# Optimization experiments

Measured on AMD Instinct MI355X. Metric: run time of the kernel, lower is better.

Reference implementation:

```python
import jax, jax.numpy as jnp
import numpy as np

N_NODE, N_PRICE, N_CB, N_CM = 50000, 100, 50, 500
EMB, NNZ, LAYERS = 128, 1_000_000, 2


def setup_inputs() -> dict:
    key = jax.random.key(0)
    ks = iter(jax.random.split(key, 64))
    f = lambda shape: jax.random.normal(next(ks), shape, dtype=jnp.float32)
    u = lambda shape: jax.random.uniform(next(ks), shape, dtype=jnp.float32)
    inp = {
        'adj_indices': jax.random.randint(next(ks), (2, NNZ), 0, N_NODE),
        'adj_values': u((NNZ,)),
        'adjacency_pv': u((N_PRICE, N_NODE)),
        'adjacency_vp': u((N_NODE, N_PRICE)),
        'adjacency_pcb': u((N_PRICE, N_CB)),
        'adjacency_cbp': u((N_CB, N_PRICE)),
        'adjacency_cbv': u((N_CB, N_NODE)),
        'adjacency_vcb': u((N_NODE, N_CB)),
        'adjacency_pcm': u((N_PRICE, N_CM)),
        'adjacency_cmp': u((N_CM, N_PRICE)),
        'adjacency_cmv': u((N_CM, N_NODE)),
        'adjacency_vcm': u((N_NODE, N_CM)),
        'adjacency_cbcm': u((N_CB, N_CM)),
        'adjacency_cmcb': u((N_CM, N_CB)),
        'item_emb': f((N_NODE, EMB)) * 0.1,
        'pri_emb': f((N_PRICE, EMB)) * 0.1,
        'cateBig_emb': f((N_CB, EMB)) * 0.1,
        'cateMiddle_emb': f((N_CM, EMB)) * 0.1,
        'mat_vp': f((N_NODE, 1)), 'mat_vcb': f((N_NODE, 1)), 'mat_vcm': f((N_NODE, 1)),
        'mat_pv': f((N_PRICE, 1)), 'mat_pcb': f((N_PRICE, 1)), 'mat_pcm': f((N_PRICE, 1)),
        'mat_cbp': f((N_CB, 1)), 'mat_cbv': f((N_CB, 1)), 'mat_cbcm': f((N_CB, 1)),
        'mat_cmp': f((N_CM, 1)), 'mat_cmv': f((N_CM, 1)), 'mat_cmcb': f((N_CM, 1)),
        'Wi': f((EMB, 1)) * 0.1, 'bi': jnp.zeros((1,), jnp.float32),
        'Wp': f((EMB, 1)) * 0.1, 'bp': jnp.zeros((1,), jnp.float32),
        'Wcb': f((EMB, 1)) * 0.1, 'bcb': jnp.zeros((1,), jnp.float32),
        'Wcm': f((EMB, 1)) * 0.1, 'bcm': jnp.zeros((1,), jnp.float32),
    }
    return inp


def _intra_gate(dense_adj, mat_v, emb2):
    # original: alpha = softmax(mm(expand(mat_v), emb2^T)) == softmax(mat_v * rowsum(emb2))
    s = jnp.sum(emb2, axis=1)               # [m]
    alpha = jax.nn.softmax(mat_v * s[None, :], axis=1)  # [n,m] (mat_v is [n,1])
    alpha = alpha * dense_adj
    alpha = alpha / (jnp.sum(alpha, axis=1, keepdims=True) + 1e-8)
    return alpha @ emb2                      # [n,emb]  (dropout70 omitted: eval mode)


def _inter_gate(W, b, e0, e1, e2, e3):
    embs = (e0, e1, e2, e3)
    scores = [jnp.exp(e @ W + b) for e in embs]   # each [n,1]
    tot = scores[0] + scores[1] + scores[2] + scores[3]
    out = sum((s / tot) * e for s, e in zip(scores, embs))
    return out                               # (dropout50 omitted: eval mode)


def _spmm(indices, values, emb, num_rows):
    # sparse COO adjacency @ emb : out[row] += val * emb[col]
    return jax.ops.segment_sum(values[:, None] * emb[indices[1]], indices[0],
                               num_segments=num_rows)


def reference(adj_indices, adj_values,
              adjacency_pv, adjacency_vp, adjacency_pcb, adjacency_cbp,
              adjacency_cbv, adjacency_vcb, adjacency_pcm, adjacency_cmp,
              adjacency_cmv, adjacency_vcm, adjacency_cbcm, adjacency_cmcb,
              item_emb, pri_emb, cateBig_emb, cateMiddle_emb,
              mat_vp, mat_vcb, mat_vcm, mat_pv, mat_pcb, mat_pcm,
              mat_cbp, mat_cbv, mat_cbcm, mat_cmp, mat_cmv, mat_cmcb,
              Wi, bi, Wp, bp, Wcb, bcb, Wcm, bcm):
    for _ in range(LAYERS):
        item_new = _inter_gate(Wi, bi, item_emb,
                               _intra_gate(adjacency_vp, mat_vp, pri_emb),
                               _intra_gate(adjacency_vcb, mat_vcb, cateBig_emb),
                               _intra_gate(adjacency_vcm, mat_vcm, cateMiddle_emb)) \
                   + _spmm(adj_indices, adj_values, item_emb, N_NODE)
        pri_new = _inter_gate(Wp, bp, pri_emb,
                              _intra_gate(adjacency_pv, mat_pv, item_emb),
                              _intra_gate(adjacency_pcb, mat_pcb, cateBig_emb),
                              _intra_gate(adjacency_pcm, mat_pcm, cateMiddle_emb))
        cb_new = _inter_gate(Wcb, bcb, cateBig_emb,
                             _intra_gate(adjacency_cbp, mat_cbp, pri_emb),
                             _intra_gate(adjacency_cbv, mat_cbv, item_emb),
                             _intra_gate(adjacency_cbcm, mat_cbcm, cateMiddle_emb))
        cm_new = _inter_gate(Wcm, bcm, cateMiddle_emb,
                             _intra_gate(adjacency_cmp, mat_cmp, pri_emb),
                             _intra_gate(adjacency_cmv, mat_cmv, item_emb),
                             _intra_gate(adjacency_cmcb, mat_cmcb, cateBig_emb))
        item_emb, pri_emb, cateBig_emb, cateMiddle_emb = item_new, pri_new, cb_new, cm_new
    return (item_emb, pri_emb)
```

## Files before the change

### kernel.cpp

```cpp
#include <hip/hip_runtime.h>

#define N_NODE 50000
#define N_PRICE 100
#define N_CB 50
#define N_CM 500
#define EMB 128
#define NNZE 1000000
#define NCH 64
#define CS2 832
#define KVPAD 53248
#define RSTRIDE 132
#define SCAN_T 1024
#define WPAD 72
#define E0P 132

typedef __attribute__((ext_vector_type(8))) short bf16x8;
typedef __attribute__((ext_vector_type(4))) float f32x4;

__device__ inline unsigned fkey(float f){
    unsigned b = __float_as_uint(f);
    return (b & 0x80000000u) ? ~b : (b | 0x80000000u);
}
__device__ inline float fdekey(unsigned k){
    unsigned b = (k & 0x80000000u) ? (k & 0x7fffffffu) : ~k;
    return __uint_as_float(b);
}
__device__ inline unsigned short f2bf(float f){
    unsigned u = __float_as_uint(f);
    u += 0x7FFFu + ((u >> 16) & 1u);
    return (unsigned short)(u >> 16);
}

__global__ __launch_bounds__(256) void k_rowsum(
    const float* __restrict__ e_v, const float* __restrict__ e_p,
    const float* __restrict__ e_cb, const float* __restrict__ e_cm,
    float* __restrict__ s_all, unsigned* __restrict__ mm)
{
    if (blockIdx.x == 0 && threadIdx.x < 8)
        mm[threadIdx.x] = (threadIdx.x & 1) ? 0u : 0xFFFFFFFFu;
    int wid  = (blockIdx.x * 256 + threadIdx.x) >> 6;
    int lane = threadIdx.x & 63;
    const int NT = N_NODE + N_PRICE + N_CB + N_CM;
    if (wid >= NT) return;
    const float* src; int lr;
    if (wid < N_NODE)                { src = e_v;  lr = wid; }
    else if (wid < N_NODE+N_PRICE)   { src = e_p;  lr = wid - N_NODE; }
    else if (wid < N_NODE+N_PRICE+N_CB){ src = e_cb; lr = wid - N_NODE - N_PRICE; }
    else                             { src = e_cm; lr = wid - N_NODE - N_PRICE - N_CB; }
    float2 v = ((const float2*)(src + (size_t)lr * EMB))[lane];
    float sum = v.x + v.y;
    #pragma unroll
    for (int o = 32; o > 0; o >>= 1) sum += __shfl_down(sum, o, 64);
    if (lane == 0) s_all[wid] = sum;
}

__global__ __launch_bounds__(256) void k_minmax(
    const float* __restrict__ s_all, unsigned* __restrict__ mm)
{
    __shared__ unsigned smin[4], smax[4];
    int t = threadIdx.x;
    if (t < 4){ smin[t] = 0xFFFFFFFFu; smax[t] = 0u; }
    __syncthreads();
    int gid = blockIdx.x * 256 + t;
    const int NT = N_NODE + N_PRICE + N_CB + N_CM;
    if (gid < NT){
        int ty = (gid < N_NODE) ? 0 :
                 (gid < N_NODE+N_PRICE) ? 1 :
                 (gid < N_NODE+N_PRICE+N_CB) ? 2 : 3;
        unsigned k = fkey(s_all[gid]);
        atomicMin(&smin[ty], k);
        atomicMax(&smax[ty], k);
    }
    __syncthreads();
    if (t < 4){
        if (smin[t] != 0xFFFFFFFFu) atomicMin(&mm[2*t],   smin[t]);
        if (smax[t] != 0u)          atomicMax(&mm[2*t+1], smax[t]);
    }
}

__global__ __launch_bounds__(256) void k_hist(
    const int* __restrict__ rows, int* __restrict__ counts)
{
    int i = blockIdx.x * 256 + threadIdx.x;
    if (i < NNZE) atomicAdd(&counts[rows[i]], 1);
}

__global__ __launch_bounds__(SCAN_T) void k_scan(
    const int* __restrict__ counts, int* __restrict__ offs, int* __restrict__ cursor)
{
    __shared__ int part[SCAN_T];
    int t = threadIdx.x;
    const int CHUNK = (N_NODE + SCAN_T - 1) / SCAN_T;
    int base = t * CHUNK;
    int s = 0;
    for (int i = 0; i < CHUNK; i++){
        int idx = base + i;
        if (idx < N_NODE) s += counts[idx];
    }
    part[t] = s;
    __syncthreads();
    for (int o = 1; o < SCAN_T; o <<= 1){
        int u = (t >= o) ? part[t - o] : 0;
        __syncthreads();
        part[t] += u;
        __syncthreads();
    }
    int run = part[t] - s;
    for (int i = 0; i < CHUNK; i++){
        int idx = base + i;
        if (idx < N_NODE){
            offs[idx] = run; cursor[idx] = run;
            run += counts[idx];
        }
    }
    if (t == SCAN_T - 1) offs[N_NODE] = run;
}

__global__ __launch_bounds__(256) void k_scatter(
    const int* __restrict__ rows, const int* __restrict__ cols,
    const float* __restrict__ vals, int* __restrict__ cursor,
    int* __restrict__ scol, float* __restrict__ sval)
{
    int i = blockIdx.x * 256 + threadIdx.x;
    if (i < NNZE){
        int r = rows[i];
        int p = atomicAdd(&cursor[r], 1);
        scol[p] = cols[i];
        sval[p] = vals[i];
    }
}

__global__ __launch_bounds__(256) void k_spmm_csr(
    const int* __restrict__ offs, const int* __restrict__ scol,
    const float* __restrict__ sval, const float* __restrict__ emb,
    float* __restrict__ out)
{
    int row  = (blockIdx.x * 256 + threadIdx.x) >> 6;
    int lane = threadIdx.x & 63;
    if (row >= N_NODE) return;
    int s = offs[row], e = offs[row + 1];
    float2 acc = make_float2(0.f, 0.f);
    for (int base = s; base < e; base += 64){
        int n = base + lane;
        int   cl = (n < e) ? scol[n] : 0;
        float vl = (n < e) ? sval[n] : 0.f;
        int m = e - base; if (m > 64) m = 64;
        for (int j = 0; j < m; j++){
            int   c = __shfl(cl, j, 64);
            float v = __shfl(vl, j, 64);
            float2 em = *(const float2*)(emb + (size_t)c * EMB + lane * 2);
            acc.x += v * em.x; acc.y += v * em.y;
        }
    }
    float* dst = out + (size_t)row * EMB + lane * 2;
    float2 o = *(float2*)dst;
    o.x += acc.x; o.y += acc.y;
    *(float2*)dst = o;
}

__global__ __launch_bounds__(256) void k_cast_et_t(
    const float* __restrict__ emb, unsigned short* __restrict__ Et,
    int K, int Kpad)
{
    __shared__ unsigned short tl[64][72];
    int k0 = blockIdx.x * 64, d0 = blockIdx.y * 64;
    int t = threadIdx.x;
    int r = t >> 2, cb = (t & 3) * 16;
    const float* src = emb + (size_t)(k0 + r) * EMB + d0 + cb;
    bool rv = (k0 + r) < K;
    #pragma unroll
    for (int q = 0; q < 4; q++){
        float4 v = rv ? ((const float4*)src)[q] : make_float4(0.f,0.f,0.f,0.f);
        tl[r][cb + q*4 + 0] = f2bf(v.x);
        tl[r][cb + q*4 + 1] = f2bf(v.y);
        tl[r][cb + q*4 + 2] = f2bf(v.z);
        tl[r][cb + q*4 + 3] = f2bf(v.w);
    }
    __syncthreads();
    unsigned short h[16];
    #pragma unroll
    for (int j = 0; j < 16; j++) h[j] = tl[cb + j][r];
    uint4* dst = (uint4*)(Et + (size_t)(d0 + r) * Kpad + k0 + cb);
    dst[0] = make_uint4(((unsigned)h[1]<<16)|h[0], ((unsigned)h[3]<<16)|h[2],
                        ((unsigned)h[5]<<16)|h[4], ((unsigned)h[7]<<16)|h[6]);
    dst[1] = make_uint4(((unsigned)h[9]<<16)|h[8], ((unsigned)h[11]<<16)|h[10],
                        ((unsigned)h[13]<<16)|h[12],((unsigned)h[15]<<16)|h[14]);
}

__device__ inline void gate_block_mfma(
    const float* __restrict__ adj, const float* __restrict__ matv,
    const unsigned short* __restrict__ Et, const float* __restrict__ s_src,
    const unsigned* __restrict__ mm2, float* __restrict__ out,
    int K, int Kpad, int nrows, int i0,
    unsigned short* sh_w, float* sh_c, float* sh_M, float* shD, float* shZ)
{
    int tid = threadIdx.x;
    if (tid < 64){
        int i = i0 + tid;
        float c = (i < nrows) ? matv[i] : 0.f;
        float smin = fdekey(mm2[0]), smax = fdekey(mm2[1]);
        sh_c[tid] = c;
        sh_M[tid] = (c >= 0.f) ? c * smax : c * smin;
    }
    __syncthreads();

    int wv = tid >> 6, lane = tid & 63;
    int half = lane >> 5, c2 = (lane & 31) * 2;
    int am = lane & 15, aq = lane >> 4;

    unsigned roff[8];
    float crow[8], Mrow[8], zacc[8], dacc[8];
    #pragma unroll
    for (int i = 0; i < 8; i++){
        int r = wv*16 + i*2 + half;
        int ir = i0 + r; if (ir >= nrows) ir = nrows - 1;
        roff[i] = (unsigned)ir * (unsigned)K;
        crow[i] = sh_c[r]; Mrow[i] = sh_M[r];
        zacc[i] = 0.f; dacc[i] = 0.f;
    }
    f32x4 acc[8];
    #pragma unroll
    for (int n = 0; n < 8; n++) acc[n] = (f32x4){0.f,0.f,0.f,0.f};

    int ntile = Kpad / 64;
    for (int t = 0; t < ntile; t++){
        int k0 = t * 64;
        bool inb = (k0 + c2) < K;
        float2 s2 = inb ? *(const float2*)&s_src[k0 + c2] : make_float2(0.f,0.f);
        float2 av[8];
        #pragma unroll
        for (int i = 0; i < 8; i++)
            av[i] = inb ? *(const float2*)&adj[roff[i] + k0 + c2]
                        : make_float2(0.f, 0.f);
        __syncthreads();
        #pragma unroll
        for (int i = 0; i < 8; i++){
            float ex = 0.f, ey = 0.f;
            if (inb){
                ex = __expf(crow[i]*s2.x - Mrow[i]);
                ey = __expf(crow[i]*s2.y - Mrow[i]);
            }
            zacc[i] += ex + ey;
            float wx = ex * av[i].x, wy = ey * av[i].y;
            dacc[i] += wx + wy;
            *(unsigned*)&sh_w[(wv*16 + i*2 + half) * WPAD + c2] =
                (unsigned)f2bf(wx) | ((unsigned)f2bf(wy) << 16);
        }
        __syncthreads();
        #pragma unroll
        for (int ks = 0; ks < 2; ks++){
            bf16x8 afrag = *(const bf16x8*)&sh_w[(wv*16 + am) * WPAD + ks*32 + aq*8];
            #pragma unroll
            for (int n = 0; n < 8; n++){
                bf16x8 bfrag = *(const bf16x8*)&Et[(size_t)(n*16 + am) * Kpad + k0 + ks*32 + aq*8];
                acc[n] = __builtin_amdgcn_mfma_f32_16x16x32_bf16(afrag, bfrag, acc[n], 0, 0, 0);
            }
        }
    }
    #pragma unroll
    for (int o = 1; o <= 16; o <<= 1)
        #pragma unroll
        for (int i = 0; i < 8; i++){
            dacc[i] += __shfl_xor(dacc[i], o, 64);
            zacc[i] += __shfl_xor(zacc[i], o, 64);
        }
    if ((lane & 31) == 0){
        #pragma unroll
        for (int i = 0; i < 8; i++){
            shD[wv*16 + i*2 + half] = dacc[i];
            shZ[wv*16 + i*2 + half] = zacc[i];
        }
    }
    __syncthreads();
    #pragma unroll
    for (int n = 0; n < 8; n++){
        #pragma unroll
        for (int r = 0; r < 4; r++){
            int rl = wv*16 + aq*4 + r;
            int i  = i0 + rl;
            if (i < nrows){
                float inv = 1.f / (shD[rl] + 1e-8f * shZ[rl]);
                out[(size_t)i * EMB + n*16 + am] = acc[n][r] * inv;
            }
        }
    }
}

struct GateJob {
    const float* adj; const float* matv; const unsigned short* Et;
    const float* s; const unsigned* mm2; float* out;
    int K, Kpad, nrows, blk0;
};
struct GateJobs { GateJob j[6]; int njobs; };

__global__ __launch_bounds__(256) void k_gate_batch(GateJobs jobs)
{
    __shared__ unsigned short sh_w[64 * WPAD];
    __shared__ float sh_c[64], sh_M[64], shD[64], shZ[64];
    int b = blockIdx.x;
    int ji = 0;
    for (int q = 1; q < jobs.njobs; q++) if (b >= jobs.j[q].blk0) ji = q;
    GateJob J = jobs.j[ji];
    gate_block_mfma(J.adj, J.matv, J.Et, J.s, J.mm2, J.out, J.K, J.Kpad,
                    J.nrows, (b - J.blk0) * 64, sh_w, sh_c, sh_M, shD, shZ);
}

struct FGate {
    const float* adj; const float* matv; const unsigned short* Et;
    const unsigned* mm2; int K, Kpad, soff;
};
struct FParams { FGate g[3]; };

__global__ __launch_bounds__(256) void k_item_fused(
    FParams P, const float* __restrict__ cv, const float* __restrict__ sseg,
    const float* __restrict__ W, const float* __restrict__ bptr,
    float* __restrict__ out)
{
    __shared__ unsigned short sh_w[64 * WPAD];
    __shared__ float sh_e0[64 * E0P];
    __shared__ float shs[672];
    __shared__ float sh_c[3][64], sh_M[3][64];
    __shared__ float shD[64], shZ[64];
    __shared__ float shWf[128];

    int tid = threadIdx.x;
    int i0  = blockIdx.x * 64;

    for (int j = tid; j < 672; j += 256) shs[j] = (j < 650) ? sseg[j] : 0.f;
    if (tid < 128) shWf[tid] = W[tid];
    if (tid < 192){
        int g = tid >> 6, r = tid & 63;
        int i = i0 + r;
        float c = (i < N_NODE) ? P.g[g].matv[i] : 0.f;
        float smin = fdekey(P.g[g].mm2[0]), smax = fdekey(P.g[g].mm2[1]);
        sh_c[g][r] = c;
        sh_M[g][r] = (c >= 0.f) ? c * smax : c * smin;
    }
    for (int f = tid; f < 64 * 32; f += 256){
        int row = f >> 5, d4 = (f & 31) * 4;
        int i = i0 + row;
        float4 v = (i < N_NODE) ? ((const float4*)(cv + (size_t)i * EMB + d4))[0]
                                : make_float4(0.f,0.f,0.f,0.f);
        ((float4*)&sh_e0[row * E0P + d4])[0] = v;
    }
    __syncthreads();

    int wv = tid >> 6, lane = tid & 63;
    int half = lane >> 5, c2 = (lane & 31) * 2;
    int am = lane & 15, aq = lane >> 4;
    float bb = bptr[0];

    float dp[4] = {0.f,0.f,0.f,0.f};
    #pragma unroll
    for (int n = 0; n < 8; n++)
        #pragma unroll
        for (int r = 0; r < 4; r++)
            dp[r] += sh_e0[(wv*16 + aq*4 + r) * E0P + n*16 + am] * shWf[n*16 + am];
    #pragma unroll
    for (int o = 1; o <= 8; o <<= 1)
        #pragma unroll
        for (int r = 0; r < 4; r++) dp[r] += __shfl_xor(dp[r], o, 64);
    float stot[4];
    #pragma unroll
    for (int r = 0; r < 4; r++) stot[r] = __expf(dp[r] + bb);
    f32x4 run[8];
    #pragma unroll
    for (int n = 0; n < 8; n++)
        #pragma unroll
        for (int r = 0; r < 4; r++)
            run[n][r] = stot[r] * sh_e0[(wv*16 + aq*4 + r) * E0P + n*16 + am];

    for (int g = 0; g < 3; g++){
        FGate G = P.g[g];
        const float* srcs = shs + G.soff;
        unsigned roff[8];
        float crow[8], Mrow[8], zacc[8], dacc[8];
        #pragma unroll
        for (int i = 0; i < 8; i++){
            int r = wv*16 + i*2 + half;
            int ir = i0 + r; if (ir >= N_NODE) ir = N_NODE - 1;
            roff[i] = (unsigned)ir * (unsigned)G.K;
            crow[i] = sh_c[g][r]; Mrow[i] = sh_M[g][r];
            zacc[i] = 0.f; dacc[i] = 0.f;
        }
        f32x4 acc[8];
        #pragma unroll
        for (int n = 0; n < 8; n++) acc[n] = (f32x4){0.f,0.f,0.f,0.f};
        int ntile = G.Kpad >> 6;

        for (int t = 0; t < ntile; t++){
            int k0 = t * 64;
            bool inb = (k0 + c2) < G.K;
            float2 s2 = *(const float2*)&srcs[k0 + c2];
            float2 av[8];
            #pragma unroll
            for (int i = 0; i < 8; i++)
                av[i] = inb ? *(const float2*)&G.adj[roff[i] + k0 + c2]
                            : make_float2(0.f, 0.f);
            __syncthreads();
            #pragma unroll
            for (int i = 0; i < 8; i++){
                float ex = 0.f, ey = 0.f;
                if (inb){
                    ex = __expf(crow[i]*s2.x - Mrow[i]);
                    ey = __expf(crow[i]*s2.y - Mrow[i]);
                }
                zacc[i] += ex + ey;
                float wx = ex * av[i].x, wy = ey * av[i].y;
                dacc[i] += wx + wy;
                *(unsigned*)&sh_w[(wv*16 + i*2 + half) * WPAD + c2] =
                    (unsigned)f2bf(wx) | ((unsigned)f2bf(wy) << 16);
            }
            __syncthreads();
            #pragma unroll
            for (int ks = 0; ks < 2; ks++){
                bf16x8 afrag = *(const bf16x8*)&sh_w[(wv*16 + am) * WPAD + ks*32 + aq*8];
                #pragma unroll
                for (int n = 0; n < 8; n++){
                    bf16x8 bfrag = *(const bf16x8*)&G.Et[(size_t)(n*16 + am) * G.Kpad + k0 + ks*32 + aq*8];
                    acc[n] = __builtin_amdgcn_mfma_f32_16x16x32_bf16(afrag, bfrag, acc[n], 0, 0, 0);
                }
            }
        }
        #pragma unroll
        for (int o = 1; o <= 16; o <<= 1)
            #pragma unroll
            for (int i = 0; i < 8; i++){
                dacc[i] += __shfl_xor(dacc[i], o, 64);
                zacc[i] += __shfl_xor(zacc[i], o, 64);
            }
        if ((lane & 31) == 0){
            #pragma unroll
            for (int i = 0; i < 8; i++){
                shD[wv*16 + i*2 + half] = dacc[i];
                shZ[wv*16 + i*2 + half] = zacc[i];
            }
        }
        __syncthreads();
        float inv[4];
        #pragma unroll
        for (int r = 0; r < 4; r++){
            int rl = wv*16 + aq*4 + r;
            inv[r] = 1.f / (shD[rl] + 1e-8f * shZ[rl]);
        }
        float dpg[4] = {0.f,0.f,0.f,0.f};
        #pragma unroll
        for (int n = 0; n < 8; n++)
            #pragma unroll
            for (int r = 0; r < 4; r++){
                acc[n][r] *= inv[r];
                dpg[r] += acc[n][r] * shWf[n*16 + am];
            }
        #pragma unroll
        for (int o = 1; o <= 8; o <<= 1)
            #pragma unroll
            for (int r = 0; r < 4; r++) dpg[r] += __shfl_xor(dpg[r], o, 64);
        #pragma unroll
        for (int r = 0; r < 4; r++){
            float sg = __expf(dpg[r] + bb);
            stot[r] += sg;
            #pragma unroll
            for (int n = 0; n < 8; n++) run[n][r] += sg * acc[n][r];
        }
    }
    float invs[4];
    #pragma unroll
    for (int r = 0; r < 4; r++) invs[r] = 1.f / stot[r];
    #pragma unroll
    for (int n = 0; n < 8; n++)
        #pragma unroll
        for (int r = 0; r < 4; r++){
            int i = i0 + wv*16 + aq*4 + r;
            if (i < N_NODE) out[(size_t)i * EMB + n*16 + am] = run[n][r] * invs[r];
        }
}

__global__ __launch_bounds__(256) void k_intra_tv_mfma(
    const float* __restrict__ adj, const float* __restrict__ matv,
    const unsigned short* __restrict__ Et, const float* __restrict__ s_v,
    const unsigned* __restrict__ mm2,
    float* __restrict__ part, int baseR, int rows)
{
    __shared__ unsigned short sh_w[64 * WPAD];
    __shared__ float sh_c[64], sh_M[64], sh_s[CS2];
    int tid = threadIdx.x;
    int rb = blockIdx.x / NCH;
    int ch = blockIdx.x % NCH;
    int r0 = rb * 64;
    if (tid < 64){
        int r = r0 + tid;
        float c = (r < rows) ? matv[r] : 0.f;
        float smin = fdekey(mm2[0]), smax = fdekey(mm2[1]);
        sh_c[tid] = c;
        sh_M[tid] = (c >= 0.f) ? c * smax : c * smin;
    }
    for (int j = tid; j < CS2; j += 256){
        int gj = ch * CS2 + j;
        sh_s[j] = (gj < N_NODE) ? s_v[gj] : 0.f;
    }
    __syncthreads();

    int wv = tid >> 6, lane = tid & 63;
    int half = lane >> 5, c2 = (lane & 31) * 2;
    int am = lane & 15, aq = lane >> 4;

    unsigned roff[8];
    float crow[8], Mrow[8], zacc[8], dacc[8];
    #pragma unroll
    for (int i = 0; i < 8; i++){
        int r = wv*16 + i*2 + half;
        int rr = r0 + r; if (rr >= rows) rr = rows - 1;
        roff[i] = (unsigned)rr * (unsigned)N_NODE;
        crow[i] = sh_c[r]; Mrow[i] = sh_M[r];
        zacc[i] = 0.f; dacc[i] = 0.f;
    }
    f32x4 acc[8];
    #pragma unroll
    for (int n = 0; n < 8; n++) acc[n] = (f32x4){0.f,0.f,0.f,0.f};

    for (int t = 0; t < CS2 / 64; t++){
        int k0g = ch * CS2 + t * 64;
        int k0l = t * 64;
        bool inb = (k0g + c2) < N_NODE;
        float2 s2 = *(const float2*)&sh_s[k0l + c2];
        float2 av[8];
        #pragma unroll
        for (int i = 0; i < 8; i++)
            av[i] = inb ? *(const float2*)&adj[roff[i] + k0g + c2]
                        : make_float2(0.f, 0.f);
        __syncthreads();
        #pragma unroll
        for (int i = 0; i < 8; i++){
            float ex = 0.f, ey = 0.f;
            if (inb){
                ex = __expf(crow[i]*s2.x - Mrow[i]);
                ey = __expf(crow[i]*s2.y - Mrow[i]);
            }
            zacc[i] += ex + ey;
            float wx = ex * av[i].x, wy = ey * av[i].y;
            dacc[i] += wx + wy;
            *(unsigned*)&sh_w[(wv*16 + i*2 + half) * WPAD + c2] =
                (unsigned)f2bf(wx) | ((unsigned)f2bf(wy) << 16);
        }
        __syncthreads();
        #pragma unroll
        for (int ks = 0; ks < 2; ks++){
            bf16x8 afrag = *(const bf16x8*)&sh_w[(wv*16 + am) * WPAD + ks*32 + aq*8];
            #pragma unroll
            for (int n = 0; n < 8; n++){
                bf16x8 bfrag = *(const bf16x8*)&Et[(size_t)(n*16 + am) * KVPAD + k0g + ks*32 + aq*8];
                acc[n] = __builtin_amdgcn_mfma_f32_16x16x32_bf16(afrag, bfrag, acc[n], 0, 0, 0);
            }
        }
    }
    #pragma unroll
    for (int o = 1; o <= 16; o <<= 1)
        #pragma unroll
        for (int i = 0; i < 8; i++){
            dacc[i] += __shfl_xor(dacc[i], o, 64);
            zacc[i] += __shfl_xor(zacc[i], o, 64);
        }
    if ((lane & 31) == 0){
        #pragma unroll
        for (int i = 0; i < 8; i++){
            int rr = r0 + wv*16 + i*2 + half;
            if (rr < rows){
                float* d2 = part + ((size_t)(baseR + rr) * NCH + ch) * RSTRIDE;
                d2[128] = dacc[i]; d2[129] = zacc[i];
            }
        }
    }
    #pragma unroll
    for (int n = 0; n < 8; n++){
        #pragma unroll
        for (int r = 0; r < 4; r++){
            int rl = wv*16 + aq*4 + r;
            int rr = r0 + rl;
            if (rr < rows){
                float* d2 = part + ((size_t)(baseR + rr) * NCH + ch) * RSTRIDE;
                d2[n*16 + am] = acc[n][r];
            }
        }
    }
}

struct RIJob {
    const float* e0; float* out; const float* gA; const float* gB;
    const float* W; const float* b; int baseR; int nrows; int row0;
};
struct RIJobs { RIJob j[3]; int njobs; };

__global__ __launch_bounds__(128) void k_reduce_inter(
    RIJobs jobs, const float* __restrict__ part)
{
    __shared__ float sh[4][EMB];
    __shared__ float shW[EMB];
    int b = blockIdx.x;
    int ji = 0;
    for (int q = 1; q < jobs.njobs; q++) if (b >= jobs.j[q].row0) ji = q;
    RIJob J = jobs.j[ji];
    int r = b - J.row0;
    int d = threadIdx.x;
    float num = 0.f, den = 0.f, Z = 0.f;
    for (int c = 0; c < NCH; c++){
        const float* p = part + ((size_t)(J.baseR + r) * NCH + c) * RSTRIDE;
        num += p[d]; den += p[128]; Z += p[129];
    }
    sh[1][d] = num / (den + 1e-8f * Z);
    sh[0][d] = J.e0[(size_t)r * EMB + d];
    sh[2][d] = J.gA[(size_t)r * EMB + d];
    sh[3][d] = J.gB[(size_t)r * EMB + d];
    shW[d] = J.W[d];
    __syncthreads();
    float dots[4];
    #pragma unroll
    for (int g = 0; g < 4; g++){
        float acc = 0.f;
        for (int k = 0; k < EMB; k++) acc += sh[g][k] * shW[k];
        dots[g] = acc;
    }
    float bb = J.b[0];
    float s0 = __expf(dots[0] + bb), s1 = __expf(dots[1] + bb);
    float s2 = __expf(dots[2] + bb), s3 = __expf(dots[3] + bb);
    float inv = 1.f / (s0 + s1 + s2 + s3);
    J.out[(size_t)r * EMB + d] =
        (s0*sh[0][d] + s1*sh[1][d] + s2*sh[2][d] + s3*sh[3][d]) * inv;
}

extern "C" void kernel_launch(void* const* d_in, const int* in_sizes, int n_in,
                              void* d_out, int out_size, void* d_ws, size_t ws_size,
                              hipStream_t stream)
{
    const int*   adj_idx  = (const int*)d_in[0];
    const float* adj_val  = (const float*)d_in[1];
    const float* a_pv   = (const float*)d_in[2];
    const float* a_vp   = (const float*)d_in[3];
    const float* a_pcb  = (const float*)d_in[4];
    const float* a_cbp  = (const float*)d_in[5];
    const float* a_cbv  = (const float*)d_in[6];
    const float* a_vcb  = (const float*)d_in[7];
    const float* a_pcm  = (const float*)d_in[8];
    const float* a_cmp  = (const float*)d_in[9];
    const float* a_cmv  = (const float*)d_in[10];
    const float* a_vcm  = (const float*)d_in[11];
    const float* a_cbcm = (const float*)d_in[12];
    const float* a_cmcb = (const float*)d_in[13];
    const float* in_item = (const float*)d_in[14];
    const float* in_pri  = (const float*)d_in[15];
    const float* in_cb   = (const float*)d_in[16];
    const float* in_cm   = (const float*)d_in[17];
    const float* m_vp  = (const float*)d_in[18];
    const float* m_vcb = (const float*)d_in[19];
    const float* m_vcm = (const float*)d_in[20];
    const float* m_pv  = (const float*)d_in[21];
    const float* m_pcb = (const float*)d_in[22];
    const float* m_pcm = (const float*)d_in[23];
    const float* m_cbp = (const float*)d_in[24];
    const float* m_cbv = (const float*)d_in[25];
    const float* m_cbcm= (const float*)d_in[26];
    const float* m_cmp = (const float*)d_in[27];
    const float* m_cmv = (const float*)d_in[28];
    const float* m_cmcb= (const float*)d_in[29];
    const float* Wi = (const float*)d_in[30]; const float* bi = (const float*)d_in[31];
    const float* Wp = (const float*)d_in[32]; const float* bp = (const float*)d_in[33];
    const float* Wcb= (const float*)d_in[34]; const float* bcb= (const float*)d_in[35];
    const float* Wcm= (const float*)d_in[36]; const float* bcm= (const float*)d_in[37];

    float* ws = (float*)d_ws;
    size_t off = 0;
    auto alloc = [&](size_t n){ float* p = ws + off; off += (n + 63) & ~(size_t)63; return p; };
    float* buf_item = alloc((size_t)N_NODE * EMB);
    float* buf_pri  = alloc((size_t)N_PRICE * EMB);
    float* buf_cb   = alloc((size_t)N_CB * EMB);
    float* buf_cm   = alloc((size_t)N_CM * EMB);
    float* s_all    = alloc(N_NODE + N_PRICE + N_CB + N_CM);
    unsigned* mm    = (unsigned*)alloc(64);
    float* g1 = alloc((size_t)N_NODE * EMB);
    float* g3 = alloc((size_t)N_NODE * EMB);
    float* part = g1;
    unsigned short* et_v = (unsigned short*)g3;
    int*   counts = (int*)alloc(N_NODE + 64);
    int*   offs   = (int*)alloc(N_NODE + 64);
    int*   cursor = (int*)alloc(N_NODE + 64);
    int*   scol   = (int*)alloc(NNZE);
    float* sval   = alloc(NNZE);
    unsigned short* et_p  = (unsigned short*)alloc(EMB * 128 / 2);
    unsigned short* et_cb = (unsigned short*)alloc(EMB * 64 / 2);
    unsigned short* et_cm = (unsigned short*)alloc(EMB * 512 / 2);
    float* g_pcb  = alloc((size_t)N_PRICE * EMB);
    float* g_pcm  = alloc((size_t)N_PRICE * EMB);
    float* g_cbp  = alloc((size_t)N_CB * EMB);
    float* g_cbcm = alloc((size_t)N_CB * EMB);
    float* g_cmp  = alloc((size_t)N_CM * EMB);
    float* g_cmcb = alloc((size_t)N_CM * EMB);

    float* out_item = (float*)d_out;
    float* out_pri  = (float*)d_out + (size_t)N_NODE * EMB;

    const float* s_v  = s_all;
    const float* s_p  = s_all + N_NODE;
    const float* s_cb = s_all + N_NODE + N_PRICE;
    const float* s_cm = s_all + N_NODE + N_PRICE + N_CB;

    const int totr = N_NODE + N_PRICE + N_CB + N_CM;

    hipMemsetAsync(counts, 0, N_NODE * sizeof(int), stream);
    k_hist<<<(NNZE + 255)/256, 256, 0, stream>>>(adj_idx, counts);
    k_scan<<<1, SCAN_T, 0, stream>>>(counts, offs, cursor);
    k_scatter<<<(NNZE + 255)/256, 256, 0, stream>>>(adj_idx, adj_idx + NNZE,
                                                    adj_val, cursor, scol, sval);

    for (int layer = 0; layer < 2; layer++){
        const float* cv  = layer ? buf_item : in_item;
        const float* cp  = layer ? buf_pri  : in_pri;
        const float* ccb = layer ? buf_cb   : in_cb;
        const float* ccm = layer ? buf_cm   : in_cm;
        float* ov = layer ? out_item : buf_item;
        float* op = layer ? out_pri  : buf_pri;

        k_rowsum<<<(totr + 3)/4, 256, 0, stream>>>(cv, cp, ccb, ccm, s_all, mm);
        k_minmax<<<(totr + 255)/256, 256, 0, stream>>>(s_all, mm);

        k_cast_et_t<<<dim3(2, 2), 256, 0, stream>>>(cp,  et_p,  N_PRICE, 128);
        k_cast_et_t<<<dim3(1, 2), 256, 0, stream>>>(ccb, et_cb, N_CB,    64);
        k_cast_et_t<<<dim3(8, 2), 256, 0, stream>>>(ccm, et_cm, N_CM,    512);

        GateJobs gj{};
        int nb = 0, nj = 0;
        auto addjob = [&](const float* adj_, const float* matv_,
                          const unsigned short* Et_, const float* s_,
                          const unsigned* mm2_, float* out_,
                          int K_, int Kpad_, int nrows_){
            gj.j[nj] = GateJob{adj_, matv_, Et_, s_, mm2_, out_,
                               K_, Kpad_, nrows_, nb};
            nb += (nrows_ + 63) / 64; nj++;
        };
        addjob(a_pcb, m_pcb, et_cb, s_cb, mm+4, g_pcb, N_CB,    64, N_PRICE);
        addjob(a_pcm, m_pcm, et_cm, s_cm, mm+6, g_pcm, N_CM,   512, N_PRICE);
        if (layer == 0){
            addjob(a_cbp,  m_cbp,  et_p,  s_p,  mm+2, g_cbp,  N_PRICE, 128, N_CB);
            addjob(a_cbcm, m_cbcm, et_cm, s_cm, mm+6, g_cbcm, N_CM,   512, N_CB);
            addjob(a_cmp,  m_cmp,  et_p,  s_p,  mm+2, g_cmp,  N_PRICE, 128, N_CM);
            addjob(a_cmcb, m_cmcb, et_cb, s_cb, mm+4, g_cmcb, N_CB,    64, N_CM);
        }
        gj.njobs = nj;
        k_gate_batch<<<nb, 256, 0, stream>>>(gj);

        FParams fp{};
        fp.g[0] = FGate{a_vp,  m_vp,  et_p,  mm+2, N_PRICE, 128, 0};
        fp.g[1] = FGate{a_vcb, m_vcb, et_cb, mm+4, N_CB,    64,  100};
        fp.g[2] = FGate{a_vcm, m_vcm, et_cm, mm+6, N_CM,    512, 150};
        k_item_fused<<<(N_NODE + 63)/64, 256, 0, stream>>>(
            fp, cv, s_all + N_NODE, Wi, bi, ov);

        k_spmm_csr<<<(N_NODE*64 + 255)/256, 256, 0, stream>>>(offs, scol, sval, cv, ov);

        k_cast_et_t<<<dim3(KVPAD/64, 2), 256, 0, stream>>>(cv, et_v, N_NODE, KVPAD);

        k_intra_tv_mfma<<<((N_PRICE + 63)/64) * NCH, 256, 0, stream>>>(
            a_pv, m_pv, et_v, s_v, mm + 0, part, 0, N_PRICE);
        if (layer == 0){
            k_intra_tv_mfma<<<((N_CB + 63)/64) * NCH, 256, 0, stream>>>(
                a_cbv, m_cbv, et_v, s_v, mm + 0, part, N_PRICE, N_CB);
            k_intra_tv_mfma<<<((N_CM + 63)/64) * NCH, 256, 0, stream>>>(
                a_cmv, m_cmv, et_v, s_v, mm + 0, part, N_PRICE + N_CB, N_CM);
        }

        RIJobs rj{};
        rj.j[0] = RIJob{cp, op, g_pcb, g_pcm, Wp, bp, 0, N_PRICE, 0};
        int nrows_tot = N_PRICE;
        int njr = 1;
        if (layer == 0){
            rj.j[1] = RIJob{ccb, buf_cb, g_cbp, g_cbcm, Wcb, bcb,
                            N_PRICE, N_CB, nrows_tot};
            nrows_tot += N_CB; njr++;
            rj.j[2] = RIJob{ccm, buf_cm, g_cmp, g_cmcb, Wcm, bcm,
                            N_PRICE + N_CB, N_CM, nrows_tot};
            nrows_tot += N_CM; njr++;
        }
        rj.njobs = njr;
        k_reduce_inter<<<nrows_tot, 128, 0, stream>>>(rj, part);
    }
    (void)in_sizes; (void)n_in; (void)out_size; (void)ws_size;
}
```

Baseline: 1.387 ms.

## Prefetch next adjacency tile into registers and drop block barriers in gate loops

In all three gate GEMM loops, the next tile's adjacency values (and source scores where applicable) are now loaded into registers before the current tile is processed. This double-buffers the global loads so their latency overlaps the exp/bf16 packing and MFMA work. The block-wide __syncthreads around the per-wave shared-memory weight tile, and the one after the row-sum reduction, are removed. This is valid because each wave reads back only the LDS rows it wrote itself. The cost is a second set of eight float2 registers per thread, which may reduce occupancy.

```diff
diff --git a/kernel.cpp b/kernel.cpp
--- a/kernel.cpp
+++ b/kernel.cpp
@@ -223,30 +223,35 @@
     for (int n = 0; n < 8; n++) acc[n] = (f32x4){0.f,0.f,0.f,0.f};
 
     int ntile = Kpad / 64;
+    float2 avC[8], avN[8], s2C, s2N;
+    bool inbC = (c2 < K), inbN;
+    s2C = inbC ? *(const float2*)&s_src[c2] : make_float2(0.f, 0.f);
+    #pragma unroll
+    for (int i = 0; i < 8; i++)
+        avC[i] = inbC ? *(const float2*)&adj[roff[i] + c2] : make_float2(0.f, 0.f);
+
     for (int t = 0; t < ntile; t++){
-        int k0 = t * 64;
-        bool inb = (k0 + c2) < K;
-        float2 s2 = inb ? *(const float2*)&s_src[k0 + c2] : make_float2(0.f,0.f);
-        float2 av[8];
+        int k0 = t * 64, k0n = k0 + 64;
+        inbN = (t + 1 < ntile) && (k0n + c2 < K);
+        s2N = inbN ? *(const float2*)&s_src[k0n + c2] : make_float2(0.f, 0.f);
         #pragma unroll
         for (int i = 0; i < 8; i++)
-            av[i] = inb ? *(const float2*)&adj[roff[i] + k0 + c2]
-                        : make_float2(0.f, 0.f);
-        __syncthreads();
+            avN[i] = inbN ? *(const float2*)&adj[roff[i] + k0n + c2]
+                          : make_float2(0.f, 0.f);
+
         #pragma unroll
         for (int i = 0; i < 8; i++){
             float ex = 0.f, ey = 0.f;
-            if (inb){
-                ex = __expf(crow[i]*s2.x - Mrow[i]);
-                ey = __expf(crow[i]*s2.y - Mrow[i]);
+            if (inbC){
+                ex = __expf(crow[i]*s2C.x - Mrow[i]);
+                ey = __expf(crow[i]*s2C.y - Mrow[i]);
             }
             zacc[i] += ex + ey;
-            float wx = ex * av[i].x, wy = ey * av[i].y;
+            float wx = ex * avC[i].x, wy = ey * avC[i].y;
             dacc[i] += wx + wy;
             *(unsigned*)&sh_w[(wv*16 + i*2 + half) * WPAD + c2] =
                 (unsigned)f2bf(wx) | ((unsigned)f2bf(wy) << 16);
         }
-        __syncthreads();
         #pragma unroll
         for (int ks = 0; ks < 2; ks++){
             bf16x8 afrag = *(const bf16x8*)&sh_w[(wv*16 + am) * WPAD + ks*32 + aq*8];
@@ -256,6 +261,9 @@
                 acc[n] = __builtin_amdgcn_mfma_f32_16x16x32_bf16(afrag, bfrag, acc[n], 0, 0, 0);
             }
         }
+        inbC = inbN; s2C = s2N;
+        #pragma unroll
+        for (int i = 0; i < 8; i++) avC[i] = avN[i];
     }
     #pragma unroll
     for (int o = 1; o <= 16; o <<= 1)
@@ -271,7 +279,6 @@
             shZ[wv*16 + i*2 + half] = zacc[i];
         }
     }
-    __syncthreads();
     #pragma unroll
     for (int n = 0; n < 8; n++){
         #pragma unroll
@@ -388,30 +395,35 @@
         for (int n = 0; n < 8; n++) acc[n] = (f32x4){0.f,0.f,0.f,0.f};
         int ntile = G.Kpad >> 6;
 
+        float2 avC[8], avN[8];
+        bool inbC = (c2 < G.K), inbN;
+        #pragma unroll
+        for (int i = 0; i < 8; i++)
+            avC[i] = inbC ? *(const float2*)&G.adj[roff[i] + c2]
+                          : make_float2(0.f, 0.f);
+
         for (int t = 0; t < ntile; t++){
-            int k0 = t * 64;
-            bool inb = (k0 + c2) < G.K;
+            int k0 = t * 64, k0n = k0 + 64;
+            inbN = (t + 1 < ntile) && (k0n + c2 < G.K);
+            #pragma unroll
+            for (int i = 0; i < 8; i++)
+                avN[i] = inbN ? *(const float2*)&G.adj[roff[i] + k0n + c2]
+                              : make_float2(0.f, 0.f);
+
             float2 s2 = *(const float2*)&srcs[k0 + c2];
-            float2 av[8];
-            #pragma unroll
-            for (int i = 0; i < 8; i++)
-                av[i] = inb ? *(const float2*)&G.adj[roff[i] + k0 + c2]
-                            : make_float2(0.f, 0.f);
-            __syncthreads();
             #pragma unroll
             for (int i = 0; i < 8; i++){
                 float ex = 0.f, ey = 0.f;
-                if (inb){
+                if (inbC){
                     ex = __expf(crow[i]*s2.x - Mrow[i]);
                     ey = __expf(crow[i]*s2.y - Mrow[i]);
                 }
                 zacc[i] += ex + ey;
-                float wx = ex * av[i].x, wy = ey * av[i].y;
+                float wx = ex * avC[i].x, wy = ey * avC[i].y;
                 dacc[i] += wx + wy;
                 *(unsigned*)&sh_w[(wv*16 + i*2 + half) * WPAD + c2] =
                     (unsigned)f2bf(wx) | ((unsigned)f2bf(wy) << 16);
             }
-            __syncthreads();
             #pragma unroll
             for (int ks = 0; ks < 2; ks++){
                 bf16x8 afrag = *(const bf16x8*)&sh_w[(wv*16 + am) * WPAD + ks*32 + aq*8];
@@ -421,6 +433,9 @@
                     acc[n] = __builtin_amdgcn_mfma_f32_16x16x32_bf16(afrag, bfrag, acc[n], 0, 0, 0);
                 }
             }
+            inbC = inbN;
+            #pragma unroll
+            for (int i = 0; i < 8; i++) avC[i] = avN[i];
         }
         #pragma unroll
         for (int o = 1; o <= 16; o <<= 1)
@@ -436,7 +451,6 @@
                 shZ[wv*16 + i*2 + half] = zacc[i];
             }
         }
-        __syncthreads();
         float inv[4];
         #pragma unroll
         for (int r = 0; r < 4; r++){
@@ -518,31 +532,37 @@
     #pragma unroll
     for (int n = 0; n < 8; n++) acc[n] = (f32x4){0.f,0.f,0.f,0.f};
 
+    float2 avC[8], avN[8];
+    bool inbC = (ch * CS2 + c2) < N_NODE, inbN;
+    #pragma unroll
+    for (int i = 0; i < 8; i++)
+        avC[i] = inbC ? *(const float2*)&adj[roff[i] + ch * CS2 + c2]
+                      : make_float2(0.f, 0.f);
+
     for (int t = 0; t < CS2 / 64; t++){
         int k0g = ch * CS2 + t * 64;
         int k0l = t * 64;
-        bool inb = (k0g + c2) < N_NODE;
+        int k0gn = k0g + 64;
+        inbN = (t + 1 < CS2 / 64) && (k0gn + c2) < N_NODE;
+        #pragma unroll
+        for (int i = 0; i < 8; i++)
+            avN[i] = inbN ? *(const float2*)&adj[roff[i] + k0gn + c2]
+                          : make_float2(0.f, 0.f);
+
         float2 s2 = *(const float2*)&sh_s[k0l + c2];
-        float2 av[8];
-        #pragma unroll
-        for (int i = 0; i < 8; i++)
-            av[i] = inb ? *(const float2*)&adj[roff[i] + k0g + c2]
-                        : make_float2(0.f, 0.f);
-        __syncthreads();
         #pragma unroll
         for (int i = 0; i < 8; i++){
             float ex = 0.f, ey = 0.f;
-            if (inb){
+            if (inbC){
                 ex = __expf(crow[i]*s2.x - Mrow[i]);
                 ey = __expf(crow[i]*s2.y - Mrow[i]);
             }
             zacc[i] += ex + ey;
-            float wx = ex * av[i].x, wy = ey * av[i].y;
+            float wx = ex * avC[i].x, wy = ey * avC[i].y;
             dacc[i] += wx + wy;
             *(unsigned*)&sh_w[(wv*16 + i*2 + half) * WPAD + c2] =
                 (unsigned)f2bf(wx) | ((unsigned)f2bf(wy) << 16);
         }
-        __syncthreads();
         #pragma unroll
         for (int ks = 0; ks < 2; ks++){
             bf16x8 afrag = *(const bf16x8*)&sh_w[(wv*16 + am) * WPAD + ks*32 + aq*8];
@@ -552,6 +572,9 @@
                 acc[n] = __builtin_amdgcn_mfma_f32_16x16x32_bf16(afrag, bfrag, acc[n], 0, 0, 0);
             }
         }
+        inbC = inbN;
+        #pragma unroll
+        for (int i = 0; i < 8; i++) avC[i] = avN[i];
     }
     #pragma unroll
     for (int o = 1; o <= 16; o <<= 1)
```

Result: faster. 1.273 ms (-8.2%).
